# Kernel tuning notes

Measured on AMD Instinct MI355X. Metric: run time of the kernel, lower is better.

## Reference

```python
import jax, jax.numpy as jnp
import numpy as np

E, C, O = 500_000, 64, 64

def setup_inputs() -> dict:
    key = jax.random.key(0)
    k1, k2, k3, k4 = jax.random.split(key, 4)
    x = jax.random.normal(k1, (E, C), dtype=jnp.float32)
    # neighbors in [-1, E): -1 marks a missing neighbor (boundary edge)
    neighbors = jax.random.randint(k2, (E, 4), -1, E, dtype=jnp.int32)
    # Linear(5C -> O): kaiming-ish init
    W = jax.random.normal(k3, (O, 5 * C), dtype=jnp.float32) * (1.0 / np.sqrt(5 * C))
    b = jax.random.normal(k4, (O,), dtype=jnp.float32) * 0.01
    return {"x": x, "neighbors": neighbors, "W": W, "b": b}

def reference(x, neighbors, W, b):
    E_, C_ = x.shape
    safe_nb = jnp.maximum(neighbors, 0)                      # clamp(min=0)
    nb_feats = x[safe_nb]                                    # [E, 4, C] gather
    missing = (neighbors < 0)[..., None]                     # [E, 4, 1]
    nb_feats = jnp.where(missing, jnp.zeros((), x.dtype), nb_feats)
    pair1 = jnp.sort(nb_feats[:, 0:2, :], axis=1)            # elementwise sort of 2
    pair2 = jnp.sort(nb_feats[:, 2:4, :], axis=1)
    combined = jnp.concatenate(
        [x, pair1.reshape(E_, 2 * C_), pair2.reshape(E_, 2 * C_)], axis=1
    )                                                         # [E, 5C]
    return combined @ W.T + b                                 # [E, O]
```

## Files before the change

### kernel.cpp

```cpp
#include <hip/hip_runtime.h>

#define E_TOT 500000
#define C_DIM 64
#define K_DIM 320

typedef __attribute__((ext_vector_type(8))) _Float16 half8;
typedef __attribute__((ext_vector_type(4))) float f32x4;

__global__ __launch_bounds__(1024)
void meshconv_kernel(const float* __restrict__ x, const int* __restrict__ nbr,
                     const float* __restrict__ W, const float* __restrict__ bias,
                     float* __restrict__ out) {
  __shared__ _Float16 Whf[20480];
  __shared__ _Float16 Wlf[20480];

  const int tid = threadIdx.x;

  for (int fidx = tid; fidx < 2560; fidx += 1024) {
    const int l   = fidx & 63;
    const int t   = (fidx >> 6) & 3;
    const int ks  = fidx >> 8;
    const int row = t * 16 + (l & 15);
    const int col = ks * 32 + (l >> 4) * 8;
    const float* src = W + row * K_DIM + col;
    float4 u = *(const float4*)(src);
    float4 v = *(const float4*)(src + 4);
    float f[8] = {u.x, u.y, u.z, u.w, v.x, v.y, v.z, v.w};
    half8 hv, lv;
#pragma unroll
    for (int j = 0; j < 8; ++j) {
      _Float16 h = (_Float16)f[j];
      hv[j] = h;
      lv[j] = (_Float16)(f[j] - (float)h);
    }
    *reinterpret_cast<half8*>(&Whf[fidx * 8]) = hv;
    *reinterpret_cast<half8*>(&Wlf[fidx * 8]) = lv;
  }
  __syncthreads();

  const int lane = tid & 63;
  const int wv   = tid >> 6;
  const int lrow = lane & 15;
  const int kc   = (lane >> 4) * 8;

  const int base = blockIdx.x * 512 + wv * 32;
  const int e0  = base + lrow;
  const int e1  = base + 16 + lrow;
  const int ec0 = min(e0, E_TOT - 1);
  const int ec1 = min(e1, E_TOT - 1);

  const int4 nb0 = *(const int4*)(nbr + ec0 * 4);
  const int4 nb1 = *(const int4*)(nbr + ec1 * 4);

  f32x4 acc[2][4];
#pragma unroll
  for (int m = 0; m < 2; ++m)
#pragma unroll
    for (int t = 0; t < 4; ++t) acc[m][t] = (f32x4){0.f, 0.f, 0.f, 0.f};

  auto load8 = [&](int row, int h, float* f) {
    const float* p = x + row * C_DIM + h * 32 + kc;
    float4 u = *(const float4*)(p);
    float4 v = *(const float4*)(p + 4);
    f[0] = u.x; f[1] = u.y; f[2] = u.z; f[3] = u.w;
    f[4] = v.x; f[5] = v.y; f[6] = v.z; f[7] = v.w;
  };
  auto cvt = [&](const float* f, half8& hv, half8& lv) {
#pragma unroll
    for (int j = 0; j < 8; ++j) {
      _Float16 h = (_Float16)f[j];
      hv[j] = h;
      lv[j] = (_Float16)(f[j] - (float)h);
    }
  };
  auto dot_step = [&](int ks, half8 ah0, half8 al0, half8 ah1, half8 al1) {
#pragma unroll
    for (int t = 0; t < 4; ++t) {
      const int off = ((ks * 4 + t) * 64 + lane) * 8;
      half8 wh = *reinterpret_cast<const half8*>(&Whf[off]);
      half8 wl = *reinterpret_cast<const half8*>(&Wlf[off]);
      acc[0][t] = __builtin_amdgcn_mfma_f32_16x16x32_f16(ah0, wh, acc[0][t], 0, 0, 0);
      acc[0][t] = __builtin_amdgcn_mfma_f32_16x16x32_f16(ah0, wl, acc[0][t], 0, 0, 0);
      acc[0][t] = __builtin_amdgcn_mfma_f32_16x16x32_f16(al0, wh, acc[0][t], 0, 0, 0);
      acc[1][t] = __builtin_amdgcn_mfma_f32_16x16x32_f16(ah1, wh, acc[1][t], 0, 0, 0);
      acc[1][t] = __builtin_amdgcn_mfma_f32_16x16x32_f16(ah1, wl, acc[1][t], 0, 0, 0);
      acc[1][t] = __builtin_amdgcn_mfma_f32_16x16x32_f16(al1, wh, acc[1][t], 0, 0, 0);
    }
  };

#pragma unroll
  for (int h = 0; h < 2; ++h) {
    float f0[8], f1[8];
    load8(ec0, h, f0);
    load8(ec1, h, f1);
    half8 ah0, al0, ah1, al1;
    cvt(f0, ah0, al0);
    cvt(f1, ah1, al1);
    dot_step(h, ah0, al0, ah1, al1);
  }

#pragma unroll
  for (int p = 0; p < 2; ++p) {
    const int nA0 = p ? nb0.z : nb0.x;
    const int nB0 = p ? nb0.w : nb0.y;
    const int nA1 = p ? nb1.z : nb1.x;
    const int nB1 = p ? nb1.w : nb1.y;
#pragma unroll
    for (int h = 0; h < 2; ++h) {
      float fa0[8], fb0[8], fa1[8], fb1[8];
      load8(max(nA0, 0), h, fa0);
      load8(max(nB0, 0), h, fb0);
      load8(max(nA1, 0), h, fa1);
      load8(max(nB1, 0), h, fb1);
      float mn0[8], mx0[8], mn1[8], mx1[8];
#pragma unroll
      for (int j = 0; j < 8; ++j) {
        float a0  = (nA0 < 0) ? 0.f : fa0[j];
        float b0v = (nB0 < 0) ? 0.f : fb0[j];
        float a1  = (nA1 < 0) ? 0.f : fa1[j];
        float b1v = (nB1 < 0) ? 0.f : fb1[j];
        mn0[j] = fminf(a0, b0v);  mx0[j] = fmaxf(a0, b0v);
        mn1[j] = fminf(a1, b1v);  mx1[j] = fmaxf(a1, b1v);
      }
      half8 mnh0, mnl0, mxh0, mxl0, mnh1, mnl1, mxh1, mxl1;
      cvt(mn0, mnh0, mnl0);  cvt(mx0, mxh0, mxl0);
      cvt(mn1, mnh1, mnl1);  cvt(mx1, mxh1, mxl1);
      dot_step(2 + 4 * p + h, mnh0, mnl0, mnh1, mnl1);
      dot_step(4 + 4 * p + h, mxh0, mxl0, mxh1, mxl1);
    }
  }

  float bv[4];
#pragma unroll
  for (int t = 0; t < 4; ++t) bv[t] = bias[t * 16 + lrow];

  const int lgrp = lane >> 4;
#pragma unroll
  for (int m = 0; m < 2; ++m)
#pragma unroll
    for (int r = 0; r < 4; ++r) {
      const int e = base + m * 16 + lgrp * 4 + r;
      if (e < E_TOT) {
        float* po = out + e * 64 + lrow;
        po[0]  = acc[m][0][r] + bv[0];
        po[16] = acc[m][1][r] + bv[1];
        po[32] = acc[m][2][r] + bv[2];
        po[48] = acc[m][3][r] + bv[3];
      }
    }
}

extern "C" void kernel_launch(void* const* d_in, const int* in_sizes, int n_in,
                              void* d_out, int out_size, void* d_ws, size_t ws_size,
                              hipStream_t stream) {
  const float* x   = (const float*)d_in[0];
  const int*   nbr = (const int*)d_in[1];
  const float* W   = (const float*)d_in[2];
  const float* b   = (const float*)d_in[3];
  float* out = (float*)d_out;
  const int blocks = (E_TOT + 511) / 512;
  hipLaunchKernelGGL(meshconv_kernel, dim3(blocks), dim3(1024), 0, stream,
                     x, nbr, W, b, out);
}
```

Baseline: 300.7 us.

## Drop split-fp16 compensation, pre-convert x to fp16 workspace, smaller blocks

Removes the hi/lo fp16 split for both W and activations, so each K-step issues one MFMA per tile instead of three and W needs half the shared memory. Adds a pre-pass that converts x to fp16 in the workspace, so neighbour gathers move half the bytes. The main kernel uses 512-thread blocks with a 4-blocks-per-CU launch bound and issues all gathers early to overlap with the MFMAs. Accuracy drops to plain fp16 inputs, which may break tolerance, and the extra conversion pass adds a full read and write of x.

```diff
diff --git a/kernel.cpp b/kernel.cpp
--- a/kernel.cpp
+++ b/kernel.cpp
@@ -2,48 +2,51 @@
 
 #define E_TOT 500000
 #define C_DIM 64
-#define K_DIM 320
 
 typedef __attribute__((ext_vector_type(8))) _Float16 half8;
 typedef __attribute__((ext_vector_type(4))) float f32x4;
 
-__global__ __launch_bounds__(1024)
-void meshconv_kernel(const float* __restrict__ x, const int* __restrict__ nbr,
-                     const float* __restrict__ W, const float* __restrict__ bias,
-                     float* __restrict__ out) {
-  __shared__ _Float16 Whf[20480];
-  __shared__ _Float16 Wlf[20480];
+__global__ __launch_bounds__(256)
+void cvt_x_kernel(const float* __restrict__ x, _Float16* __restrict__ x16) {
+  const size_t i = (size_t)blockIdx.x * 256 + threadIdx.x;
+  const float4* src = (const float4*)x + 2 * i;
+  float4 u = src[0], v = src[1];
+  half8 h;
+  h[0] = (_Float16)u.x; h[1] = (_Float16)u.y; h[2] = (_Float16)u.z; h[3] = (_Float16)u.w;
+  h[4] = (_Float16)v.x; h[5] = (_Float16)v.y; h[6] = (_Float16)v.z; h[7] = (_Float16)v.w;
+  *((half8*)x16 + i) = h;
+}
+
+template <bool USE16>
+__global__ __launch_bounds__(512, 4)
+void meshconv_main(const float* __restrict__ x, const _Float16* __restrict__ x16,
+                   const int* __restrict__ nbr, const float* __restrict__ W,
+                   const float* __restrict__ bias, float* __restrict__ out) {
+  __shared__ _Float16 Wh[20480];
 
   const int tid = threadIdx.x;
-
-  for (int fidx = tid; fidx < 2560; fidx += 1024) {
+  for (int fidx = tid; fidx < 2560; fidx += 512) {
     const int l   = fidx & 63;
     const int t   = (fidx >> 6) & 3;
     const int ks  = fidx >> 8;
     const int row = t * 16 + (l & 15);
     const int col = ks * 32 + (l >> 4) * 8;
-    const float* src = W + row * K_DIM + col;
-    float4 u = *(const float4*)(src);
+    const float* src = W + row * 320 + col;
+    float4 u = *(const float4*)src;
     float4 v = *(const float4*)(src + 4);
-    float f[8] = {u.x, u.y, u.z, u.w, v.x, v.y, v.z, v.w};
-    half8 hv, lv;
-#pragma unroll
-    for (int j = 0; j < 8; ++j) {
-      _Float16 h = (_Float16)f[j];
-      hv[j] = h;
-      lv[j] = (_Float16)(f[j] - (float)h);
-    }
-    *reinterpret_cast<half8*>(&Whf[fidx * 8]) = hv;
-    *reinterpret_cast<half8*>(&Wlf[fidx * 8]) = lv;
+    half8 h;
+    h[0] = (_Float16)u.x; h[1] = (_Float16)u.y; h[2] = (_Float16)u.z; h[3] = (_Float16)u.w;
+    h[4] = (_Float16)v.x; h[5] = (_Float16)v.y; h[6] = (_Float16)v.z; h[7] = (_Float16)v.w;
+    *reinterpret_cast<half8*>(&Wh[fidx * 8]) = h;
   }
   __syncthreads();
 
   const int lane = tid & 63;
   const int wv   = tid >> 6;
   const int lrow = lane & 15;
-  const int kc   = (lane >> 4) * 8;
+  const int kc8  = (lane >> 4) * 8;
 
-  const int base = blockIdx.x * 512 + wv * 32;
+  const int base = blockIdx.x * 256 + wv * 32;
   const int e0  = base + lrow;
   const int e1  = base + 16 + lrow;
   const int ec0 = min(e0, E_TOT - 1);
@@ -58,76 +61,80 @@
 #pragma unroll
     for (int t = 0; t < 4; ++t) acc[m][t] = (f32x4){0.f, 0.f, 0.f, 0.f};
 
-  auto load8 = [&](int row, int h, float* f) {
-    const float* p = x + row * C_DIM + h * 32 + kc;
-    float4 u = *(const float4*)(p);
-    float4 v = *(const float4*)(p + 4);
-    f[0] = u.x; f[1] = u.y; f[2] = u.z; f[3] = u.w;
-    f[4] = v.x; f[5] = v.y; f[6] = v.z; f[7] = v.w;
-  };
-  auto cvt = [&](const float* f, half8& hv, half8& lv) {
-#pragma unroll
-    for (int j = 0; j < 8; ++j) {
-      _Float16 h = (_Float16)f[j];
-      hv[j] = h;
-      lv[j] = (_Float16)(f[j] - (float)h);
-    }
-  };
-  auto dot_step = [&](int ks, half8 ah0, half8 al0, half8 ah1, half8 al1) {
-#pragma unroll
-    for (int t = 0; t < 4; ++t) {
-      const int off = ((ks * 4 + t) * 64 + lane) * 8;
-      half8 wh = *reinterpret_cast<const half8*>(&Whf[off]);
-      half8 wl = *reinterpret_cast<const half8*>(&Wlf[off]);
-      acc[0][t] = __builtin_amdgcn_mfma_f32_16x16x32_f16(ah0, wh, acc[0][t], 0, 0, 0);
-      acc[0][t] = __builtin_amdgcn_mfma_f32_16x16x32_f16(ah0, wl, acc[0][t], 0, 0, 0);
-      acc[0][t] = __builtin_amdgcn_mfma_f32_16x16x32_f16(al0, wh, acc[0][t], 0, 0, 0);
-      acc[1][t] = __builtin_amdgcn_mfma_f32_16x16x32_f16(ah1, wh, acc[1][t], 0, 0, 0);
-      acc[1][t] = __builtin_amdgcn_mfma_f32_16x16x32_f16(ah1, wl, acc[1][t], 0, 0, 0);
-      acc[1][t] = __builtin_amdgcn_mfma_f32_16x16x32_f16(al1, wh, acc[1][t], 0, 0, 0);
+  auto gat = [&](int row, int h) -> half8 {
+    if constexpr (USE16) {
+      return *reinterpret_cast<const half8*>(x16 + (size_t)row * 64 + h * 32 + kc8);
+    } else {
+      const float* p = x + (size_t)row * 64 + h * 32 + kc8;
+      float4 u = *(const float4*)p;
+      float4 v = *(const float4*)(p + 4);
+      half8 r;
+      r[0] = (_Float16)u.x; r[1] = (_Float16)u.y; r[2] = (_Float16)u.z; r[3] = (_Float16)u.w;
+      r[4] = (_Float16)v.x; r[5] = (_Float16)v.y; r[6] = (_Float16)v.z; r[7] = (_Float16)v.w;
+      return r;
     }
   };
 
+  auto mnmx = [&](half8 a, half8 b, int na, int nb_, half8& mn, half8& mx) {
+    const half8 zero = (half8)(_Float16)0.0f;
+    if (na < 0)  a = zero;
+    if (nb_ < 0) b = zero;
+    mn = __builtin_elementwise_min(a, b);
+    mx = __builtin_elementwise_max(a, b);
+  };
+
+  auto dot2 = [&](int ks, half8 a0, half8 a1) {
 #pragma unroll
-  for (int h = 0; h < 2; ++h) {
-    float f0[8], f1[8];
-    load8(ec0, h, f0);
-    load8(ec1, h, f1);
-    half8 ah0, al0, ah1, al1;
-    cvt(f0, ah0, al0);
-    cvt(f1, ah1, al1);
-    dot_step(h, ah0, al0, ah1, al1);
+    for (int t = 0; t < 4; ++t) {
+      half8 w = *reinterpret_cast<const half8*>(&Wh[((ks * 4 + t) * 64 + lane) * 8]);
+      acc[0][t] = __builtin_amdgcn_mfma_f32_16x16x32_f16(a0, w, acc[0][t], 0, 0, 0);
+      acc[1][t] = __builtin_amdgcn_mfma_f32_16x16x32_f16(a1, w, acc[1][t], 0, 0, 0);
+    }
+  };
+
+  const int r0a = max(nb0.x, 0), r0b = max(nb0.y, 0);
+  const int r1a = max(nb1.x, 0), r1b = max(nb1.y, 0);
+  const int r0c = max(nb0.z, 0), r0d = max(nb0.w, 0);
+  const int r1c = max(nb1.z, 0), r1d = max(nb1.w, 0);
+
+  half8 o00 = gat(ec0, 0), o01 = gat(ec0, 1);
+  half8 o10 = gat(ec1, 0), o11 = gat(ec1, 1);
+
+  half8 a00 = gat(r0a, 0), b00 = gat(r0b, 0);
+  half8 a10 = gat(r1a, 0), b10 = gat(r1b, 0);
+  half8 a01 = gat(r0a, 1), b01 = gat(r0b, 1);
+  half8 a11 = gat(r1a, 1), b11 = gat(r1b, 1);
+
+  dot2(0, o00, o10);
+  dot2(1, o01, o11);
+
+  half8 c00 = gat(r0c, 0), d00 = gat(r0d, 0);
+  half8 c10 = gat(r1c, 0), d10 = gat(r1d, 0);
+  half8 c01 = gat(r0c, 1), d01 = gat(r0d, 1);
+  half8 c11 = gat(r1c, 1), d11 = gat(r1d, 1);
+
+  {
+    half8 mn0, mx0, mn1, mx1;
+    mnmx(a00, b00, nb0.x, nb0.y, mn0, mx0);
+    mnmx(a10, b10, nb1.x, nb1.y, mn1, mx1);
+    dot2(2, mn0, mn1);
+    dot2(4, mx0, mx1);
+    mnmx(a01, b01, nb0.x, nb0.y, mn0, mx0);
+    mnmx(a11, b11, nb1.x, nb1.y, mn1, mx1);
+    dot2(3, mn0, mn1);
+    dot2(5, mx0, mx1);
   }
 
-#pragma unroll
-  for (int p = 0; p < 2; ++p) {
-    const int nA0 = p ? nb0.z : nb0.x;
-    const int nB0 = p ? nb0.w : nb0.y;
-    const int nA1 = p ? nb1.z : nb1.x;
-    const int nB1 = p ? nb1.w : nb1.y;
-#pragma unroll
-    for (int h = 0; h < 2; ++h) {
-      float fa0[8], fb0[8], fa1[8], fb1[8];
-      load8(max(nA0, 0), h, fa0);
-      load8(max(nB0, 0), h, fb0);
-      load8(max(nA1, 0), h, fa1);
-      load8(max(nB1, 0), h, fb1);
-      float mn0[8], mx0[8], mn1[8], mx1[8];
-#pragma unroll
-      for (int j = 0; j < 8; ++j) {
-        float a0  = (nA0 < 0) ? 0.f : fa0[j];
-        float b0v = (nB0 < 0) ? 0.f : fb0[j];
-        float a1  = (nA1 < 0) ? 0.f : fa1[j];
-        float b1v = (nB1 < 0) ? 0.f : fb1[j];
-        mn0[j] = fminf(a0, b0v);  mx0[j] = fmaxf(a0, b0v);
-        mn1[j] = fminf(a1, b1v);  mx1[j] = fmaxf(a1, b1v);
-      }
-      half8 mnh0, mnl0, mxh0, mxl0, mnh1, mnl1, mxh1, mxl1;
-      cvt(mn0, mnh0, mnl0);  cvt(mx0, mxh0, mxl0);
-      cvt(mn1, mnh1, mnl1);  cvt(mx1, mxh1, mxl1);
-      dot_step(2 + 4 * p + h, mnh0, mnl0, mnh1, mnl1);
-      dot_step(4 + 4 * p + h, mxh0, mxl0, mxh1, mxl1);
-    }
+  {
+    half8 mn0, mx0, mn1, mx1;
+    mnmx(c00, d00, nb0.z, nb0.w, mn0, mx0);
+    mnmx(c10, d10, nb1.z, nb1.w, mn1, mx1);
+    dot2(6, mn0, mn1);
+    dot2(8, mx0, mx1);
+    mnmx(c01, d01, nb0.z, nb0.w, mn0, mx0);
+    mnmx(c11, d11, nb1.z, nb1.w, mn1, mx1);
+    dot2(7, mn0, mn1);
+    dot2(9, mx0, mx1);
   }
 
   float bv[4];
@@ -141,7 +148,7 @@
     for (int r = 0; r < 4; ++r) {
       const int e = base + m * 16 + lgrp * 4 + r;
       if (e < E_TOT) {
-        float* po = out + e * 64 + lrow;
+        float* po = out + (size_t)e * 64 + lrow;
         po[0]  = acc[m][0][r] + bv[0];
         po[16] = acc[m][1][r] + bv[1];
         po[32] = acc[m][2][r] + bv[2];
@@ -158,7 +165,18 @@
   const float* W   = (const float*)d_in[2];
   const float* b   = (const float*)d_in[3];
   float* out = (float*)d_out;
-  const int blocks = (E_TOT + 511) / 512;
-  hipLaunchKernelGGL(meshconv_kernel, dim3(blocks), dim3(1024), 0, stream,
-                     x, nbr, W, b, out);
+
+  const int mblocks = (E_TOT + 255) / 256;
+  const size_t need = (size_t)E_TOT * C_DIM * sizeof(_Float16);
+
+  if (ws_size >= need) {
+    _Float16* x16 = (_Float16*)d_ws;
+    const int cblocks = (E_TOT * C_DIM) / (256 * 8);
+    hipLaunchKernelGGL(cvt_x_kernel, dim3(cblocks), dim3(256), 0, stream, x, x16);
+    hipLaunchKernelGGL((meshconv_main<true>), dim3(mblocks), dim3(512), 0, stream,
+                       x, x16, nbr, W, b, out);
+  } else {
+    hipLaunchKernelGGL((meshconv_main<false>), dim3(mblocks), dim3(512), 0, stream,
+                       x, (const _Float16*)nullptr, nbr, W, b, out);
+  }
 }
```

New measurement: 298.2 us. No clear change (-0.8%).
